# Performance work log

Hardware: AMD Instinct MI355X
Metric: run time of the kernel (lower is better)

## Reference

```python
import jax, jax.numpy as jnp
import numpy as np

N, E = 50000, 1_000_000
IN_F, OUT_F = 128, 64
NEG_SLOPE = 0.2


def setup_inputs() -> dict:
    key = jax.random.key(0)
    k1, k2, k3, k4, k5 = jax.random.split(key, 5)
    x = jax.random.normal(k1, (N, IN_F), dtype=jnp.float32)
    edge_index = jax.random.randint(k2, (2, E), 0, N, dtype=jnp.int64)
    # xavier_uniform with gain=1.414 (as in the torch init)
    gain = 1.414
    bW = gain * np.sqrt(6.0 / (IN_F + OUT_F))
    W = jax.random.uniform(k3, (IN_F, OUT_F), jnp.float32, -bW, bW)
    ba = gain * np.sqrt(6.0 / (OUT_F + 1))
    a_src = jax.random.uniform(k4, (OUT_F, 1), jnp.float32, -ba, ba)
    a_dst = jax.random.uniform(k5, (OUT_F, 1), jnp.float32, -ba, ba)
    return {"x": x, "edge_index": edge_index, "W": W, "a_src": a_src, "a_dst": a_dst}


def reference(x, edge_index, W, a_src, a_dst):
    n = x.shape[0]
    Wh = x @ W                                  # [N, F_out]
    src = edge_index[0]
    dst = edge_index[1]
    # per-edge attention logits: (Wh[src] . a_src) + (Wh[dst] . a_dst)
    s_src = Wh @ a_src[:, 0]                    # [N]
    s_dst = Wh @ a_dst[:, 0]                    # [N]
    e = jax.nn.leaky_relu(s_src[src] + s_dst[dst], negative_slope=NEG_SLOPE)  # [E]
    e = jnp.exp(e - jnp.max(e))                 # global-max stabilized exp (matches torch code)
    denom = jax.ops.segment_sum(e, dst, num_segments=n) + 1e-16  # [N]
    alpha = e / denom[dst]                      # [E]  (dropout p=0 -> identity)
    out = jax.ops.segment_sum(Wh[src] * alpha[:, None], dst, num_segments=n)  # [N, F_out]
    return jax.nn.elu(out)
```

## Files before the change

kernel.cpp:

```cpp
#include <hip/hip_runtime.h>
#include <hip/hip_bf16.h>
#include <math.h>

#define NN 50000
#define NE 1000000
#define FIN 128
#define FOUT 64
#define NEG 0.2f

#define NB   2048
#define DPB  25
#define NBUSED 2000
#define TS   4096
#define NT   245
#define NTP  256
#define TILE_BLKS 245
#define GEMM_BLKS 391

using short8  = __attribute__((ext_vector_type(8))) short;
using floatx4 = __attribute__((ext_vector_type(4))) float;

static __device__ __forceinline__ short f2bf(float f) {
    __hip_bfloat16 h = __float2bfloat16(f);
    return *(short*)&h;
}

__global__ __launch_bounds__(512) void k_front(
    const float* __restrict__ x, const float* __restrict__ W,
    const float* __restrict__ a_src, const float* __restrict__ a_dst,
    const int* __restrict__ ei,
    __hip_bfloat16* __restrict__ Whb, float* __restrict__ s_src,
    float* __restrict__ s_dst,
    unsigned* __restrict__ bdata, int* __restrict__ gofs)
{
    __shared__ int cnt[NB];
    __shared__ int cur[NB];
    __shared__ unsigned srt[TS];
    __shared__ int wsum[8];

    const int tid  = threadIdx.x;
    const int lane = tid & 63;
    const int wv   = tid >> 6;

    if (blockIdx.x >= TILE_BLKS) {
        const int col  = lane & 15;
        const int quad = lane >> 4;
        const int strip = (blockIdx.x - TILE_BLKS) * 8 + wv;
        if (strip >= NN / 16) return;
        const int row0 = strip * 16;

        short8 bfr[4][4];
        #pragma unroll
        for (int kk = 0; kk < 4; ++kk) {
            #pragma unroll
            for (int nt = 0; nt < 4; ++nt) {
                const float* wp = W + (kk * 32 + quad * 8) * FOUT + nt * 16 + col;
                #pragma unroll
                for (int j = 0; j < 8; ++j)
                    bfr[kk][nt][j] = f2bf(wp[j * FOUT]);
            }
        }

        floatx4 acc[4] = {{0.f,0.f,0.f,0.f},{0.f,0.f,0.f,0.f},
                          {0.f,0.f,0.f,0.f},{0.f,0.f,0.f,0.f}};

        const float* xrow = x + (size_t)(row0 + col) * FIN + quad * 8;
        #pragma unroll
        for (int kk = 0; kk < 4; ++kk) {
            const float4 u0 = *(const float4*)(xrow + kk * 32);
            const float4 u1 = *(const float4*)(xrow + kk * 32 + 4);
            short8 af;
            af[0] = f2bf(u0.x); af[1] = f2bf(u0.y);
            af[2] = f2bf(u0.z); af[3] = f2bf(u0.w);
            af[4] = f2bf(u1.x); af[5] = f2bf(u1.y);
            af[6] = f2bf(u1.z); af[7] = f2bf(u1.w);
            #pragma unroll
            for (int nt = 0; nt < 4; ++nt)
                acc[nt] = __builtin_amdgcn_mfma_f32_16x16x32_bf16(
                    af, bfr[kk][nt], acc[nt], 0, 0, 0);
        }

        const float av0 = a_src[col], av1 = a_src[16 + col];
        const float av2 = a_src[32 + col], av3 = a_src[48 + col];
        const float bv0 = a_dst[col], bv1 = a_dst[16 + col];
        const float bv2 = a_dst[32 + col], bv3 = a_dst[48 + col];

        float ps[4], pd[4];
        #pragma unroll
        for (int reg = 0; reg < 4; ++reg) {
            ps[reg] = acc[0][reg] * av0 + acc[1][reg] * av1
                    + acc[2][reg] * av2 + acc[3][reg] * av3;
            pd[reg] = acc[0][reg] * bv0 + acc[1][reg] * bv1
                    + acc[2][reg] * bv2 + acc[3][reg] * bv3;
        }

        #pragma unroll
        for (int nt = 0; nt < 4; ++nt)
            #pragma unroll
            for (int reg = 0; reg < 4; ++reg)
                Whb[(size_t)(row0 + quad * 4 + reg) * FOUT + nt * 16 + col] =
                    __float2bfloat16(acc[nt][reg]);

        #pragma unroll
        for (int off = 1; off < 16; off <<= 1) {
            #pragma unroll
            for (int reg = 0; reg < 4; ++reg) {
                ps[reg] += __shfl_xor(ps[reg], off);
                pd[reg] += __shfl_xor(pd[reg], off);
            }
        }
        if (col == 0) {
            #pragma unroll
            for (int reg = 0; reg < 4; ++reg) {
                s_src[row0 + quad * 4 + reg] = ps[reg];
                s_dst[row0 + quad * 4 + reg] = pd[reg];
            }
        }
        return;
    }

    const int tile = blockIdx.x;
    const int base = tile * TS;
    const int tcnt = (NE - base < TS) ? (NE - base) : TS;

    for (int i = tid; i < NB; i += 512) cnt[i] = 0;
    __syncthreads();

    unsigned pk[8];
    #pragma unroll
    for (int j = 0; j < 8; ++j) {
        const int i = j * 512 + tid;
        if (i < tcnt) {
            const int e = base + i;
            const unsigned s = (unsigned)__builtin_nontemporal_load(ei + e);
            const unsigned d = (unsigned)__builtin_nontemporal_load(ei + NE + e);
            pk[j] = (s << 16) | d;
            atomicAdd(&cnt[d / DPB], 1);
        } else pk[j] = 0xFFFFFFFFu;
    }
    __syncthreads();

    {
        const int i0 = tid * 4;
        const int v0 = cnt[i0], v1 = cnt[i0 + 1];
        const int v2 = cnt[i0 + 2], v3 = cnt[i0 + 3];
        const int s = v0 + v1 + v2 + v3;
        int inc = s;
        #pragma unroll
        for (int off = 1; off < 64; off <<= 1) {
            const int t = __shfl_up(inc, off);
            if (lane >= off) inc += t;
        }
        if (lane == 63) wsum[wv] = inc;
        __syncthreads();
        int wb = 0;
        #pragma unroll
        for (int w = 0; w < 7; ++w) if (w < wv) wb += wsum[w];
        const int excl = wb + inc - s;
        cur[i0]     = excl;
        cur[i0 + 1] = excl + v0;
        cur[i0 + 2] = excl + v0 + v1;
        cur[i0 + 3] = excl + v0 + v1 + v2;
        *(int4*)(gofs + (size_t)tile * NB + i0) =
            make_int4(excl, excl + v0, excl + v0 + v1, excl + v0 + v1 + v2);
    }
    __syncthreads();

    #pragma unroll
    for (int j = 0; j < 8; ++j) {
        if (pk[j] != 0xFFFFFFFFu) {
            const int b = (int)(pk[j] & 0xffffu) / DPB;
            const int pos = atomicAdd(&cur[b], 1);
            srt[pos] = pk[j];
        }
    }
    __syncthreads();

    for (int i = tid; i < tcnt; i += 512)
        bdata[base + i] = srt[i];
}

__global__ __launch_bounds__(256) void k_transp(
    const int* __restrict__ gofs, int* __restrict__ gofs_t)
{
    __shared__ int tb[32][33];
    const int bi = blockIdx.x & 63;
    const int ti = blockIdx.x >> 6;
    const int r = threadIdx.x >> 5;
    const int c = threadIdx.x & 31;
    for (int rr = r; rr < 32; rr += 8) {
        const int t = ti * 32 + rr;
        tb[rr][c] = (t < NT) ? gofs[(size_t)t * NB + bi * 32 + c] : 0;
    }
    __syncthreads();
    for (int rr = r; rr < 32; rr += 8) {
        const int b = bi * 32 + rr;
        gofs_t[(size_t)b * NTP + ti * 32 + c] = tb[c][rr];
    }
}

__global__ __launch_bounds__(256) void k_sortgather(
    const int* __restrict__ gofs_t, const unsigned* __restrict__ bdata,
    const float* __restrict__ s_src, const float* __restrict__ s_dst,
    const __hip_bfloat16* __restrict__ Whb, float* __restrict__ out)
{
    __shared__ unsigned raw[1024];
    __shared__ unsigned srt[1024];
    __shared__ float evs[1024];
    __shared__ float sdl[32];
    __shared__ int cnt[32];
    __shared__ int ofs2[33];
    __shared__ int cur[32];
    __shared__ int wsum[4];

    const int b = (blockIdx.x & 7) * (NBUSED / 8) + (blockIdx.x >> 3);
    const int tid = threadIdx.x;
    const int lane = tid & 63;
    const int wv = tid >> 6;
    const int d0 = b * DPB;

    if (tid < 32) {
        cnt[tid] = 0;
        sdl[tid] = (tid < DPB) ? s_dst[d0 + tid] : 0.f;
    }

    int c = 0, o = 0;
    if (tid < NT) {
        o = gofs_t[(size_t)b * NTP + tid];
        c = gofs_t[(size_t)(b + 1) * NTP + tid] - o;
    }
    int inc = c;
    #pragma unroll
    for (int off = 1; off < 64; off <<= 1) {
        const int t = __shfl_up(inc, off);
        if (lane >= off) inc += t;
    }
    if (lane == 63) wsum[wv] = inc;
    __syncthreads();
    int wb = 0;
    #pragma unroll
    for (int w = 0; w < 3; ++w) if (w < wv) wb += wsum[w];
    const int segbase = wb + inc - c;
    const int tot = wsum[0] + wsum[1] + wsum[2] + wsum[3];

    for (int k = 0; k < c; ++k)
        raw[segbase + k] = bdata[(size_t)tid * TS + o + k];
    __syncthreads();

    for (int i = tid; i < tot; i += 256)
        atomicAdd(&cnt[(int)(raw[i] & 0xffffu) - d0], 1);
    __syncthreads();

    if (tid < 32) {
        const int cc = (tid < DPB) ? cnt[tid] : 0;
        int in2 = cc;
        #pragma unroll
        for (int off = 1; off < 32; off <<= 1) {
            const int t = __shfl_up(in2, off);
            if (tid >= off) in2 += t;
        }
        ofs2[tid + 1] = in2;
        if (tid == 0) ofs2[0] = 0;
        cur[tid] = in2 - cc;
    }
    __syncthreads();

    for (int i = tid; i < tot; i += 256) {
        const unsigned p = raw[i];
        const int j = (int)(p & 0xffffu) - d0;
        const int pos = atomicAdd(&cur[j], 1);
        srt[pos] = p;
        float v = s_src[p >> 16] + sdl[j];
        v = (v > 0.f) ? v : NEG * v;
        evs[pos] = __expf(v);
    }
    __syncthreads();

    for (int j = wv; j < DPB; j += 4) {
        const int d = d0 + j;
        const int beg = ofs2[j];
        const int end = ofs2[j + 1];
        float acc = 0.f, den = 0.f;
        int i = beg;
        for (; i + 8 <= end; i += 8) {
            int ss[8]; float ee[8], w[8];
            #pragma unroll
            for (int k = 0; k < 8; ++k) {
                ss[k] = (int)(srt[i + k] >> 16);
                ee[k] = evs[i + k];
            }
            #pragma unroll
            for (int k = 0; k < 8; ++k)
                w[k] = __bfloat162float(Whb[(size_t)ss[k] * FOUT + lane]);
            #pragma unroll
            for (int k = 0; k < 8; ++k) {
                acc = fmaf(ee[k], w[k], acc);
                den += ee[k];
            }
        }
        for (; i < end; ++i) {
            const int s0 = (int)(srt[i] >> 16);
            const float e0 = evs[i];
            acc = fmaf(e0, __bfloat162float(Whb[(size_t)s0 * FOUT + lane]), acc);
            den += e0;
        }
        const float r = acc / (den + 1e-16f);
        out[(size_t)d * FOUT + lane] = (r > 0.f) ? r : expm1f(r);
    }
}

extern "C" void kernel_launch(void* const* d_in, const int* in_sizes, int n_in,
                              void* d_out, int out_size, void* d_ws, size_t ws_size,
                              hipStream_t stream)
{
    const float* x     = (const float*)d_in[0];
    const int*   ei    = (const int*)d_in[1];
    const float* W     = (const float*)d_in[2];
    const float* a_src = (const float*)d_in[3];
    const float* a_dst = (const float*)d_in[4];
    float* out = (float*)d_out;

    float* ws    = (float*)d_ws;
    __hip_bfloat16* Whb = (__hip_bfloat16*)ws;
    float* s_src = ws + (size_t)NN * FOUT / 2;
    float* s_dst = s_src + NN;
    int*   gofs  = (int*)(s_dst + NN);
    int*   gofs_t = gofs + (size_t)NT * NB;
    unsigned* bdata = (unsigned*)(gofs_t + (size_t)NB * NTP);

    k_front<<<TILE_BLKS + GEMM_BLKS, 512, 0, stream>>>(
        x, W, a_src, a_dst, ei, Whb, s_src, s_dst, bdata, gofs);
    k_transp<<<512, 256, 0, stream>>>(gofs, gofs_t);
    k_sortgather<<<NBUSED, 256, 0, stream>>>(gofs_t, bdata, s_src, s_dst,
                                             Whb, out);
}
```

Measured before the change: 123.8 us.

## Use coarser destination buckets of 100 nodes with 512-thread sortgather blocks

Cuts the number of destination buckets from 2048 to 512, so each bucket covers 100 nodes instead of 25. This shrinks the per-tile offset table, the transpose, and the per-bucket segment reads in the gather kernel. The gather kernel now runs 512 threads per block on larger shared-memory bucket buffers capped at 2560 entries. The cap silently drops edges if a bucket ever exceeds it, which is a correctness risk for skewed inputs. Fewer, larger blocks also change occupancy and raise LDS usage per block.

```diff
diff --git a/kernel.cpp b/kernel.cpp
--- a/kernel.cpp
+++ b/kernel.cpp
@@ -8,12 +8,13 @@
 #define FOUT 64
 #define NEG 0.2f
 
-#define NB   2048
-#define DPB  25
-#define NBUSED 2000
+#define NB   512
+#define DPB  100
+#define NBUSED 500
 #define TS   4096
 #define NT   245
 #define NTP  256
+#define RCAP 2560
 #define TILE_BLKS 245
 #define GEMM_BLKS 391
 
@@ -123,7 +124,7 @@
     const int base = tile * TS;
     const int tcnt = (NE - base < TS) ? (NE - base) : TS;
 
-    for (int i = tid; i < NB; i += 512) cnt[i] = 0;
+    if (tid < NB) cnt[tid] = 0;
     __syncthreads();
 
     unsigned pk[8];
@@ -141,11 +142,8 @@
     __syncthreads();
 
     {
-        const int i0 = tid * 4;
-        const int v0 = cnt[i0], v1 = cnt[i0 + 1];
-        const int v2 = cnt[i0 + 2], v3 = cnt[i0 + 3];
-        const int s = v0 + v1 + v2 + v3;
-        int inc = s;
+        const int v = cnt[tid];
+        int inc = v;
         #pragma unroll
         for (int off = 1; off < 64; off <<= 1) {
             const int t = __shfl_up(inc, off);
@@ -156,13 +154,9 @@
         int wb = 0;
         #pragma unroll
         for (int w = 0; w < 7; ++w) if (w < wv) wb += wsum[w];
-        const int excl = wb + inc - s;
-        cur[i0]     = excl;
-        cur[i0 + 1] = excl + v0;
-        cur[i0 + 2] = excl + v0 + v1;
-        cur[i0 + 3] = excl + v0 + v1 + v2;
-        *(int4*)(gofs + (size_t)tile * NB + i0) =
-            make_int4(excl, excl + v0, excl + v0 + v1, excl + v0 + v1 + v2);
+        const int excl = wb + inc - v;
+        cur[tid] = excl;
+        gofs[(size_t)tile * NB + tid] = excl;
     }
     __syncthreads();
 
@@ -184,8 +178,8 @@
     const int* __restrict__ gofs, int* __restrict__ gofs_t)
 {
     __shared__ int tb[32][33];
-    const int bi = blockIdx.x & 63;
-    const int ti = blockIdx.x >> 6;
+    const int bi = blockIdx.x & 15;
+    const int ti = blockIdx.x >> 4;
     const int r = threadIdx.x >> 5;
     const int c = threadIdx.x & 31;
     for (int rr = r; rr < 32; rr += 8) {
@@ -199,30 +193,29 @@
     }
 }
 
-__global__ __launch_bounds__(256) void k_sortgather(
+__global__ __launch_bounds__(512) void k_sortgather(
     const int* __restrict__ gofs_t, const unsigned* __restrict__ bdata,
     const float* __restrict__ s_src, const float* __restrict__ s_dst,
     const __hip_bfloat16* __restrict__ Whb, float* __restrict__ out)
 {
-    __shared__ unsigned raw[1024];
-    __shared__ unsigned srt[1024];
-    __shared__ float evs[1024];
-    __shared__ float sdl[32];
-    __shared__ int cnt[32];
-    __shared__ int ofs2[33];
-    __shared__ int cur[32];
-    __shared__ int wsum[4];
-
-    const int b = (blockIdx.x & 7) * (NBUSED / 8) + (blockIdx.x >> 3);
+    __shared__ unsigned raw[RCAP];
+    __shared__ unsigned srt[RCAP];
+    __shared__ float evs[RCAP];
+    __shared__ float sdl[DPB];
+    __shared__ int cnt[128];
+    __shared__ int ofs2[129];
+    __shared__ int cur[128];
+    __shared__ int wsum[8];
+
+    const int b = (blockIdx.x & 7) * 64 + (blockIdx.x >> 3);
+    if (b >= NBUSED) return;
     const int tid = threadIdx.x;
     const int lane = tid & 63;
     const int wv = tid >> 6;
     const int d0 = b * DPB;
 
-    if (tid < 32) {
-        cnt[tid] = 0;
-        sdl[tid] = (tid < DPB) ? s_dst[d0 + tid] : 0.f;
-    }
+    if (tid < 128) cnt[tid] = 0;
+    if (tid < DPB) sdl[tid] = s_dst[d0 + tid];
 
     int c = 0, o = 0;
     if (tid < NT) {
@@ -239,33 +232,43 @@
     __syncthreads();
     int wb = 0;
     #pragma unroll
-    for (int w = 0; w < 3; ++w) if (w < wv) wb += wsum[w];
+    for (int w = 0; w < 7; ++w) if (w < wv) wb += wsum[w];
     const int segbase = wb + inc - c;
-    const int tot = wsum[0] + wsum[1] + wsum[2] + wsum[3];
-
-    for (int k = 0; k < c; ++k)
-        raw[segbase + k] = bdata[(size_t)tid * TS + o + k];
-    __syncthreads();
-
-    for (int i = tid; i < tot; i += 256)
+    int tot = 0;
+    #pragma unroll
+    for (int w = 0; w < 8; ++w) tot += wsum[w];
+    if (tot > RCAP) tot = RCAP;
+
+    for (int k = 0; k < c; ++k) {
+        const int p = segbase + k;
+        if (p < RCAP) raw[p] = bdata[(size_t)tid * TS + o + k];
+    }
+    __syncthreads();
+
+    for (int i = tid; i < tot; i += 512)
         atomicAdd(&cnt[(int)(raw[i] & 0xffffu) - d0], 1);
     __syncthreads();
 
-    if (tid < 32) {
-        const int cc = (tid < DPB) ? cnt[tid] : 0;
-        int in2 = cc;
-        #pragma unroll
-        for (int off = 1; off < 32; off <<= 1) {
+    if (tid < 64) {
+        const int c0 = cnt[2 * tid];
+        const int c1 = cnt[2 * tid + 1];
+        const int s = c0 + c1;
+        int in2 = s;
+        #pragma unroll
+        for (int off = 1; off < 64; off <<= 1) {
             const int t = __shfl_up(in2, off);
             if (tid >= off) in2 += t;
         }
-        ofs2[tid + 1] = in2;
-        if (tid == 0) ofs2[0] = 0;
-        cur[tid] = in2 - cc;
-    }
-    __syncthreads();
-
-    for (int i = tid; i < tot; i += 256) {
+        const int excl = in2 - s;
+        ofs2[2 * tid]     = excl;
+        ofs2[2 * tid + 1] = excl + c0;
+        cur[2 * tid]      = excl;
+        cur[2 * tid + 1]  = excl + c0;
+        if (tid == 63) ofs2[128] = in2;
+    }
+    __syncthreads();
+
+    for (int i = tid; i < tot; i += 512) {
         const unsigned p = raw[i];
         const int j = (int)(p & 0xffffu) - d0;
         const int pos = atomicAdd(&cur[j], 1);
@@ -276,7 +279,7 @@
     }
     __syncthreads();
 
-    for (int j = wv; j < DPB; j += 4) {
+    for (int j = wv; j < DPB; j += 8) {
         const int d = d0 + j;
         const int beg = ofs2[j];
         const int end = ofs2[j + 1];
@@ -325,12 +328,12 @@
     float* s_src = ws + (size_t)NN * FOUT / 2;
     float* s_dst = s_src + NN;
     int*   gofs  = (int*)(s_dst + NN);
-    int*   gofs_t = gofs + (size_t)NT * NB;
+    int*   gofs_t = gofs + (size_t)256 * NB;
     unsigned* bdata = (unsigned*)(gofs_t + (size_t)NB * NTP);
 
     k_front<<<TILE_BLKS + GEMM_BLKS, 512, 0, stream>>>(
         x, W, a_src, a_dst, ei, Whb, s_src, s_dst, bdata, gofs);
-    k_transp<<<512, 256, 0, stream>>>(gofs, gofs_t);
-    k_sortgather<<<NBUSED, 256, 0, stream>>>(gofs_t, bdata, s_src, s_dst,
-                                             Whb, out);
-}
+    k_transp<<<128, 256, 0, stream>>>(gofs, gofs_t);
+    k_sortgather<<<512, 512, 0, stream>>>(gofs_t, bdata, s_src, s_dst,
+                                          Whb, out);
+}
```

Result: slower. 135.3 us (+9.4%).

## Scatter edges into padded per-bucket slabs via global atomics, drop transpose kernel

Applied to the files above, without the earlier changes.

Instead of writing each tile's locally sorted edges contiguously along with a per-tile offset table, which then had to be transposed, the front kernel reserves space in a fixed-capacity slab per destination bucket using a global atomic counter. It writes each edge directly into that slab. The gather kernel then reads one contiguous slab per bucket, and the transpose kernel is removed in favour of a small memset. Buckets are doubled to 50 destinations each, and the gather kernel now runs 512-thread blocks. Edges beyond the fixed slab capacity of 1280 are silently dropped, so correctness relies on the roughly uniform degree distribution of the inputs.

```diff
diff --git a/kernel.cpp b/kernel.cpp
--- a/kernel.cpp
+++ b/kernel.cpp
@@ -8,12 +8,11 @@
 #define FOUT 64
 #define NEG 0.2f
 
-#define NB   2048
-#define DPB  25
-#define NBUSED 2000
-#define TS   4096
-#define NT   245
-#define NTP  256
+#define NB     1024
+#define DPB    50
+#define NBUSED 1000
+#define TS     4096
+#define PADCAP 1280
 #define TILE_BLKS 245
 #define GEMM_BLKS 391
 
@@ -31,10 +30,12 @@
     const int* __restrict__ ei,
     __hip_bfloat16* __restrict__ Whb, float* __restrict__ s_src,
     float* __restrict__ s_dst,
-    unsigned* __restrict__ bdata, int* __restrict__ gofs)
+    int* __restrict__ bcur, unsigned* __restrict__ bdata2)
 {
     __shared__ int cnt[NB];
+    __shared__ int ofs[NB];
     __shared__ int cur[NB];
+    __shared__ int gpos[NB];
     __shared__ unsigned srt[TS];
     __shared__ int wsum[8];
 
@@ -123,7 +124,7 @@
     const int base = tile * TS;
     const int tcnt = (NE - base < TS) ? (NE - base) : TS;
 
-    for (int i = tid; i < NB; i += 512) cnt[i] = 0;
+    cnt[tid] = 0; cnt[tid + 512] = 0;
     __syncthreads();
 
     unsigned pk[8];
@@ -141,10 +142,9 @@
     __syncthreads();
 
     {
-        const int i0 = tid * 4;
+        const int i0 = tid * 2;
         const int v0 = cnt[i0], v1 = cnt[i0 + 1];
-        const int v2 = cnt[i0 + 2], v3 = cnt[i0 + 3];
-        const int s = v0 + v1 + v2 + v3;
+        const int s = v0 + v1;
         int inc = s;
         #pragma unroll
         for (int off = 1; off < 64; off <<= 1) {
@@ -157,12 +157,10 @@
         #pragma unroll
         for (int w = 0; w < 7; ++w) if (w < wv) wb += wsum[w];
         const int excl = wb + inc - s;
-        cur[i0]     = excl;
-        cur[i0 + 1] = excl + v0;
-        cur[i0 + 2] = excl + v0 + v1;
-        cur[i0 + 3] = excl + v0 + v1 + v2;
-        *(int4*)(gofs + (size_t)tile * NB + i0) =
-            make_int4(excl, excl + v0, excl + v0 + v1, excl + v0 + v1 + v2);
+        ofs[i0]     = excl;      ofs[i0 + 1] = excl + v0;
+        cur[i0]     = excl;      cur[i0 + 1] = excl + v0;
+        if (v0 > 0) gpos[i0]     = i0 * PADCAP + atomicAdd(&bcur[i0], v0);
+        if (v1 > 0) gpos[i0 + 1] = (i0 + 1) * PADCAP + atomicAdd(&bcur[i0 + 1], v1);
     }
     __syncthreads();
 
@@ -176,86 +174,52 @@
     }
     __syncthreads();
 
-    for (int i = tid; i < tcnt; i += 512)
-        bdata[base + i] = srt[i];
-}
-
-__global__ __launch_bounds__(256) void k_transp(
-    const int* __restrict__ gofs, int* __restrict__ gofs_t)
-{
-    __shared__ int tb[32][33];
-    const int bi = blockIdx.x & 63;
-    const int ti = blockIdx.x >> 6;
-    const int r = threadIdx.x >> 5;
-    const int c = threadIdx.x & 31;
-    for (int rr = r; rr < 32; rr += 8) {
-        const int t = ti * 32 + rr;
-        tb[rr][c] = (t < NT) ? gofs[(size_t)t * NB + bi * 32 + c] : 0;
-    }
-    __syncthreads();
-    for (int rr = r; rr < 32; rr += 8) {
-        const int b = bi * 32 + rr;
-        gofs_t[(size_t)b * NTP + ti * 32 + c] = tb[c][rr];
-    }
-}
-
-__global__ __launch_bounds__(256) void k_sortgather(
-    const int* __restrict__ gofs_t, const unsigned* __restrict__ bdata,
+    for (int i = tid; i < tcnt; i += 512) {
+        const unsigned p = srt[i];
+        const int bb = (int)(p & 0xffffu) / DPB;
+        const int dpos = gpos[bb] + (i - ofs[bb]);
+        if (dpos < (bb + 1) * PADCAP) bdata2[dpos] = p;
+    }
+}
+
+__global__ __launch_bounds__(512) void k_sortgather(
+    const int* __restrict__ bcur, const unsigned* __restrict__ bdata2,
     const float* __restrict__ s_src, const float* __restrict__ s_dst,
     const __hip_bfloat16* __restrict__ Whb, float* __restrict__ out)
 {
-    __shared__ unsigned raw[1024];
-    __shared__ unsigned srt[1024];
-    __shared__ float evs[1024];
-    __shared__ float sdl[32];
-    __shared__ int cnt[32];
-    __shared__ int ofs2[33];
-    __shared__ int cur[32];
-    __shared__ int wsum[4];
-
-    const int b = (blockIdx.x & 7) * (NBUSED / 8) + (blockIdx.x >> 3);
+    __shared__ unsigned raw[PADCAP];
+    __shared__ unsigned srt[PADCAP];
+    __shared__ float evs[PADCAP];
+    __shared__ float sdl[DPB];
+    __shared__ int cnt[64];
+    __shared__ int ofs2[65];
+    __shared__ int cur[64];
+
+    const int b = blockIdx.x;
     const int tid = threadIdx.x;
     const int lane = tid & 63;
     const int wv = tid >> 6;
     const int d0 = b * DPB;
 
-    if (tid < 32) {
-        cnt[tid] = 0;
-        sdl[tid] = (tid < DPB) ? s_dst[d0 + tid] : 0.f;
-    }
-
-    int c = 0, o = 0;
-    if (tid < NT) {
-        o = gofs_t[(size_t)b * NTP + tid];
-        c = gofs_t[(size_t)(b + 1) * NTP + tid] - o;
-    }
-    int inc = c;
-    #pragma unroll
-    for (int off = 1; off < 64; off <<= 1) {
-        const int t = __shfl_up(inc, off);
-        if (lane >= off) inc += t;
-    }
-    if (lane == 63) wsum[wv] = inc;
-    __syncthreads();
-    int wb = 0;
-    #pragma unroll
-    for (int w = 0; w < 3; ++w) if (w < wv) wb += wsum[w];
-    const int segbase = wb + inc - c;
-    const int tot = wsum[0] + wsum[1] + wsum[2] + wsum[3];
-
-    for (int k = 0; k < c; ++k)
-        raw[segbase + k] = bdata[(size_t)tid * TS + o + k];
-    __syncthreads();
-
-    for (int i = tid; i < tot; i += 256)
+    if (tid < 64) cnt[tid] = 0;
+    if (tid < DPB) sdl[tid] = s_dst[d0 + tid];
+
+    int tot = bcur[b];
+    if (tot > PADCAP) tot = PADCAP;
+    const unsigned* slab = bdata2 + (size_t)b * PADCAP;
+
+    for (int i = tid; i < tot; i += 512) raw[i] = slab[i];
+    __syncthreads();
+
+    for (int i = tid; i < tot; i += 512)
         atomicAdd(&cnt[(int)(raw[i] & 0xffffu) - d0], 1);
     __syncthreads();
 
-    if (tid < 32) {
+    if (tid < 64) {
         const int cc = (tid < DPB) ? cnt[tid] : 0;
         int in2 = cc;
         #pragma unroll
-        for (int off = 1; off < 32; off <<= 1) {
+        for (int off = 1; off < 64; off <<= 1) {
             const int t = __shfl_up(in2, off);
             if (tid >= off) in2 += t;
         }
@@ -265,7 +229,7 @@
     }
     __syncthreads();
 
-    for (int i = tid; i < tot; i += 256) {
+    for (int i = tid; i < tot; i += 512) {
         const unsigned p = raw[i];
         const int j = (int)(p & 0xffffu) - d0;
         const int pos = atomicAdd(&cur[j], 1);
@@ -276,7 +240,7 @@
     }
     __syncthreads();
 
-    for (int j = wv; j < DPB; j += 4) {
+    for (int j = wv; j < DPB; j += 8) {
         const int d = d0 + j;
         const int beg = ofs2[j];
         const int end = ofs2[j + 1];
@@ -324,13 +288,12 @@
     __hip_bfloat16* Whb = (__hip_bfloat16*)ws;
     float* s_src = ws + (size_t)NN * FOUT / 2;
     float* s_dst = s_src + NN;
-    int*   gofs  = (int*)(s_dst + NN);
-    int*   gofs_t = gofs + (size_t)NT * NB;
-    unsigned* bdata = (unsigned*)(gofs_t + (size_t)NB * NTP);
-
+    int*   bcur  = (int*)(s_dst + NN);
+    unsigned* bdata2 = (unsigned*)(bcur + NB);
+
+    hipMemsetAsync(bcur, 0, NB * sizeof(int), stream);
     k_front<<<TILE_BLKS + GEMM_BLKS, 512, 0, stream>>>(
-        x, W, a_src, a_dst, ei, Whb, s_src, s_dst, bdata, gofs);
-    k_transp<<<512, 256, 0, stream>>>(gofs, gofs_t);
-    k_sortgather<<<NBUSED, 256, 0, stream>>>(gofs_t, bdata, s_src, s_dst,
+        x, W, a_src, a_dst, ei, Whb, s_src, s_dst, bcur, bdata2);
+    k_sortgather<<<NBUSED, 512, 0, stream>>>(bcur, bdata2, s_src, s_dst,
                                              Whb, out);
 }
```

Result: slower. 129.9 us (+4.9%).
